# Kernel tuning notes

Hardware: AMD Instinct MI355X
Metric: run time of the kernel (lower is better)

Reference implementation:

```python
import jax, jax.numpy as jnp
import numpy as np

ADJ = (1, 3, 5)
GROUPS = 32


def band_mask(a, T):
    i = jnp.arange(T)
    return (jnp.abs(i[:, None] - i[None, :]) <= a).astype(jnp.float32)


def conv1d(x, w, b, groups=1, padding=0):
    # x: [N, C, T], w: [O, C//groups, K]
    out = jax.lax.conv_general_dilated(
        x, w, (1,), [(padding, padding)],
        dimension_numbers=('NCH', 'OIH', 'NCH'),
        feature_group_count=groups)
    return out + b[None, :, None]


def prslot_block(x, wp, bp, wk, bk, wa, ba, a):
    # x_adj = x[..., None].repeat(T) has identical columns; proj (1x1) and
    # region_key_conv (kernel (2a+1, 1)) act only along rows, so compute them
    # as 1D convs and broadcast at the mask multiply (same math as torch).
    T = x.shape[-1]
    h = conv1d(x, wp, bp)                 # [N, hid, T]
    k = conv1d(h, wk, bk, padding=a)      # [N, 128, T]
    km = k[:, :, :, None] * band_mask(a, T)  # [N, 128, T, T]
    # aggregate_conv: kernel (2a+1, 1) -> conv over rows only
    out = jax.lax.conv_general_dilated(
        km, wa[:, :, :, None], (1, 1), [(a, a), (0, 0)],
        dimension_numbers=('NCHW', 'OIHW', 'NCHW'))
    out = out[:, 0] + ba[0]               # [N, T, T]
    return jax.nn.softmax(out, axis=-2)   # softmax over rows (dim -2)


def setup_inputs() -> dict:
    key = jax.random.key(0)
    ks = iter(jax.random.split(key, 64))
    N, Cin, T = 8, 512, 192
    hid, cout = 256, 256

    def p(shape, scale):
        return jax.random.normal(next(ks), shape, jnp.float32) * scale

    d = {'x': jax.random.normal(next(ks), (N, Cin, T), jnp.float32)}
    for s, a in enumerate(ADJ):
        K = 2 * a + 1
        d[f'wp{s}'] = p((hid, Cin, 1), 0.02)
        d[f'bp{s}'] = jnp.zeros((hid,), jnp.float32)
        d[f'wk{s}'] = p((128, hid, K), 0.02)
        d[f'bk{s}'] = jnp.zeros((128,), jnp.float32)
        d[f'wa{s}'] = p((1, 128, K), 0.05)
        d[f'ba{s}'] = jnp.zeros((1,), jnp.float32)
    d['w1'] = p((hid, Cin, 1), 0.02)
    d['b1'] = jnp.zeros((hid,), jnp.float32)
    d['w2'] = p((hid, hid // GROUPS, 3), 0.05)
    d['b2'] = jnp.zeros((hid,), jnp.float32)
    d['w3'] = p((cout, hid, 1), 0.05)
    d['b3'] = jnp.zeros((cout,), jnp.float32)
    return d


def reference(x, wp0, bp0, wk0, bk0, wa0, ba0,
              wp1, bp1, wk1, bk1, wa1, ba1,
              wp2, bp2, wk2, bk2, wa2, ba2,
              w1, b1, w2, b2, w3, b3):
    scale_params = ((wp0, bp0, wk0, bk0, wa0, ba0),
                    (wp1, bp1, wk1, bk1, wa1, ba1),
                    (wp2, bp2, wk2, bk2, wa2, ba2))
    A = prslot_block(x, *scale_params[0], ADJ[0])
    A = A + prslot_block(x, *scale_params[1], ADJ[1])
    A = A + prslot_block(x, *scale_params[2], ADJ[2])  # [N, T, T]
    h = conv1d(x, w1, b1)
    h = jax.nn.relu(conv1d(h, w2, b2, groups=GROUPS, padding=1))
    xs = conv1d(h, w3, b3)                # [N, out, T]
    return xs @ A, A
```

## Files before the change

kernel.cpp:

```cpp
#include <hip/hip_runtime.h>

#define T_LEN 192

template<bool TRANSX>
__device__ __forceinline__ void gemm_body(
    float* smem,
    const float* __restrict__ W, const float* __restrict__ B,
    const float* __restrict__ X, float* __restrict__ Y,
    int cin, int cstr, int ostr, int wnstr,
    int t0, int o0, int n, int tid)
{
  float (*Ws)[68] = (float(*)[68])smem;
  float (*Xs)[68] = (float(*)[68])(smem + 64 * 68);
  const int to = tid >> 4, tt = tid & 15;
  float acc[4][4] = {};

  for (int c0 = 0; c0 < cin; c0 += 64) {
    __syncthreads();
#pragma unroll
    for (int l = 0; l < 4; ++l) {
      int idx = l * 256 + tid;
      int rr = idx >> 4, c4 = idx & 15;
      float4 wv = *reinterpret_cast<const float4*>(
          &W[(size_t)n * wnstr + (size_t)(o0 + rr) * cin + c0 + c4 * 4]);
      Ws[c4 * 4 + 0][rr] = wv.x; Ws[c4 * 4 + 1][rr] = wv.y;
      Ws[c4 * 4 + 2][rr] = wv.z; Ws[c4 * 4 + 3][rr] = wv.w;
      if (!TRANSX) {
        float4 xv = *reinterpret_cast<const float4*>(
            &X[((size_t)n * cstr + c0 + rr) * T_LEN + t0 + c4 * 4]);
        *reinterpret_cast<float4*>(&Xs[rr][c4 * 4]) = xv;
      } else {
        float4 xv = *reinterpret_cast<const float4*>(
            &X[((size_t)n * 192 + t0 + rr) * 192 + c0 + c4 * 4]);
        Xs[c4 * 4 + 0][rr] = xv.x; Xs[c4 * 4 + 1][rr] = xv.y;
        Xs[c4 * 4 + 2][rr] = xv.z; Xs[c4 * 4 + 3][rr] = xv.w;
      }
    }
    __syncthreads();
#pragma unroll
    for (int kk = 0; kk < 64; ++kk) {
      float4 a = *reinterpret_cast<const float4*>(&Ws[kk][to * 4]);
      float4 b = *reinterpret_cast<const float4*>(&Xs[kk][tt * 4]);
      acc[0][0] += a.x * b.x; acc[0][1] += a.x * b.y; acc[0][2] += a.x * b.z; acc[0][3] += a.x * b.w;
      acc[1][0] += a.y * b.x; acc[1][1] += a.y * b.y; acc[1][2] += a.y * b.z; acc[1][3] += a.y * b.w;
      acc[2][0] += a.z * b.x; acc[2][1] += a.z * b.y; acc[2][2] += a.z * b.z; acc[2][3] += a.z * b.w;
      acc[3][0] += a.w * b.x; acc[3][1] += a.w * b.y; acc[3][2] += a.w * b.z; acc[3][3] += a.w * b.w;
    }
  }
#pragma unroll
  for (int i = 0; i < 4; ++i) {
    float bi = B ? B[o0 + to * 4 + i] : 0.f;
    float4 v = make_float4(acc[i][0] + bi, acc[i][1] + bi, acc[i][2] + bi, acc[i][3] + bi);
    *reinterpret_cast<float4*>(
        &Y[((size_t)n * ostr + o0 + to * 4 + i) * T_LEN + t0 + tt * 4]) = v;
  }
}

template<int K, int JN>
__device__ __forceinline__ void foldA_body(
    const float* __restrict__ wa, const float* __restrict__ wk,
    float* __restrict__ parts, int j0, int chunk, int tid)
{
  float acc[JN][K];
#pragma unroll
  for (int jj = 0; jj < JN; ++jj)
#pragma unroll
    for (int i = 0; i < K; ++i) acc[jj][i] = 0.f;

  const int c0 = chunk * 16;
  for (int c = c0; c < c0 + 16; ++c) {
    const float* base = &wk[((size_t)c * 256 + tid) * K];
    float v[K];
#pragma unroll
    for (int i = 0; i < K; ++i) v[i] = base[i];
    float w[JN];
#pragma unroll
    for (int jj = 0; jj < JN; ++jj) w[jj] = wa[c * K + j0 + jj];
#pragma unroll
    for (int jj = 0; jj < JN; ++jj)
#pragma unroll
      for (int i = 0; i < K; ++i) acc[jj][i] += w[jj] * v[i];
  }
#pragma unroll
  for (int jj = 0; jj < JN; ++jj)
#pragma unroll
    for (int i = 0; i < K; ++i)
      parts[((size_t)chunk * K * K + (j0 + jj) * K + i) * 256 + tid] = acc[jj][i];
}

__device__ __forceinline__ void cka_body(
    const float* __restrict__ wa0, const float* __restrict__ bk0,
    const float* __restrict__ wa1, const float* __restrict__ bk1,
    const float* __restrict__ wa2, const float* __restrict__ bk2,
    float* __restrict__ cka, int tid)
{
  if (tid >= 21) return;
  int s, j, K; const float *wa, *bk;
  if (tid < 3)       { s = 0; j = tid;      K = 3;  wa = wa0; bk = bk0; }
  else if (tid < 10) { s = 1; j = tid - 3;  K = 7;  wa = wa1; bk = bk1; }
  else               { s = 2; j = tid - 10; K = 11; wa = wa2; bk = bk2; }
  float acc = 0.f;
  for (int c = 0; c < 128; ++c) acc += wa[c * K + j] * bk[c];
  cka[s * 11 + j] = acc;
}

template<int K>
__device__ __forceinline__ void foldB_body(
    float* lds, const float* __restrict__ parts, const float* __restrict__ wp,
    const float* __restrict__ bp, float* __restrict__ wxas,
    float* __restrict__ bpA_s, int ji, int half, int tid)
{
  constexpr int KP = (K + 3) & ~3;
  constexpr int K2 = K * K;
  float s = 0.f;
#pragma unroll
  for (int ch = 0; ch < 8; ++ch)
    s += parts[((size_t)(ch * K2 + ji)) * 256 + tid];
  lds[tid] = s;
  __syncthreads();

  const int cin = half * 256 + tid;
  float acc = 0.f;
  for (int c = 0; c < 256; ++c)
    acc += lds[c] * wp[(size_t)c * 512 + cin];
  const int j = ji / K, i = ji - j * K;
  wxas[(size_t)cin * K * KP + i * KP + j] = acc;

  if (half == 0 && tid == 0) {
    float b = 0.f;
    for (int c = 0; c < 256; ++c) b += lds[c] * bp[c];
    bpA_s[j * 11 + i] = b;
  }
}

template<int A>
__device__ __forceinline__ void rcomp_body(
    float* smem, const float* __restrict__ x, const float* __restrict__ WXAs,
    float* __restrict__ rps, int cc, int n, int tid)
{
  constexpr int K  = 2 * A + 1;
  constexpr int KP = (K + 3) & ~3;
  constexpr int WH = 192 + 2 * A;
  constexpr int WS = 204;
  float* Xs = smem;
  float* Wl = smem + 16 * WS;
  const int c0 = cc * 16;

  for (int idx = tid; idx < 16 * WH; idx += 256) {
    int c = idx / WH, p = idx - c * WH;
    int tau = p - A;
    Xs[c * WS + p] = (tau >= 0 && tau < 192)
        ? x[((size_t)n * 512 + c0 + c) * 192 + tau] : 0.f;
  }
  {
    const float4* wg = reinterpret_cast<const float4*>(WXAs + (size_t)c0 * K * KP);
    float4* wl = reinterpret_cast<float4*>(Wl);
    for (int idx = tid; idx < 16 * K * KP / 4; idx += 256) wl[idx] = wg[idx];
  }
  __syncthreads();

  const int w = tid >> 6, lane = tid & 63;
  const int csub = lane >> 4, tpos = lane & 15;
  const int tb = w * 48 + tpos * 3;

  float acc[K][3];
#pragma unroll
  for (int j = 0; j < K; ++j) { acc[j][0] = 0.f; acc[j][1] = 0.f; acc[j][2] = 0.f; }

#pragma unroll
  for (int c = 0; c < 4; ++c) {
    const int ch = csub * 4 + c;
    float win[K + 2];
#pragma unroll
    for (int p = 0; p < K + 2; ++p) win[p] = Xs[ch * WS + tb + p];
    const float* wr = &Wl[ch * K * KP];
#pragma unroll
    for (int i = 0; i < K; ++i) {
#pragma unroll
      for (int j = 0; j < K; ++j) {
        float wv = wr[i * KP + j];
        acc[j][0] += wv * win[i + 0];
        acc[j][1] += wv * win[i + 1];
        acc[j][2] += wv * win[i + 2];
      }
    }
  }
#pragma unroll
  for (int j = 0; j < K; ++j) {
#pragma unroll
    for (int q = 0; q < 3; ++q) {
      float v = acc[j][q];
      v += __shfl_xor(v, 16);
      v += __shfl_xor(v, 32);
      acc[j][q] = v;
    }
  }
  if (csub == 0) {
#pragma unroll
    for (int j = 0; j < K; ++j) {
      float* dst = &rps[(((size_t)n * 32 + cc) * K + j) * 192 + tb];
      dst[0] = acc[j][0]; dst[1] = acc[j][1]; dst[2] = acc[j][2];
    }
  }
}

__device__ __forceinline__ void rreduce_body(
    const float* __restrict__ rpart, const float* __restrict__ cka,
    const float* __restrict__ bpA, float* __restrict__ rbuf,
    int n, int sj, int t)
{
  if (t >= 192) return;
  const int s = sj < 3 ? 0 : sj < 10 ? 1 : 2;
  const int j = sj < 3 ? sj : sj < 10 ? sj - 3 : sj - 10;
  const int A = (s == 0) ? 1 : (s == 1) ? 3 : 5;
  const int K = 2 * A + 1;
  const int roff = (s == 0) ? 0 : (s == 1) ? 147456 : 491520;
  const float* rp = rpart + roff;
  float acc = cka[s * 11 + j];
#pragma unroll 8
  for (int cc = 0; cc < 32; ++cc)
    acc += rp[(((size_t)n * 32 + cc) * K + j) * 192 + t];
  for (int i = 0; i < K; ++i) {
    int tau = t + i - A;
    if (tau >= 0 && tau < 192) acc += bpA[s * 121 + j * 11 + i];
  }
  rbuf[((size_t)(s * 8 + n) * 11 + j) * 192 + t] = acc;
}

template<int A>
__device__ __forceinline__ float gather_val(const float* __restrict__ rs,
                                            int t, int u)
{
  constexpr int K = 2 * A + 1;
  float val = 0.f;
#pragma unroll
  for (int j = 0; j < K; ++j) {
    int tp = t + j - A;
    int d = tp - u;
    if (tp >= 0 && tp < 192 && d <= A && d >= -A) val += rs[j * 192 + tp];
  }
  return val;
}

__device__ __forceinline__ void abuild_body(
    const float* __restrict__ rbuf,
    const float* __restrict__ ba0, const float* __restrict__ ba1,
    const float* __restrict__ ba2, float* __restrict__ At,
    int ublk, int n, int tid)
{
  const int w = tid >> 6, lane = tid & 63;
  const int u = ublk * 4 + w;
  const int t0 = lane * 3;
  const float* r0 = rbuf + (size_t)(0 * 8 + n) * 11 * 192;
  const float* r1 = rbuf + (size_t)(1 * 8 + n) * 11 * 192;
  const float* r2 = rbuf + (size_t)(2 * 8 + n) * 11 * 192;
  float v0[3], v1[3], v2[3];
  const float b0 = ba0[0], b1 = ba1[0], b2 = ba2[0];
#pragma unroll
  for (int q = 0; q < 3; ++q) {
    v0[q] = b0 + gather_val<1>(r0, t0 + q, u);
    v1[q] = b1 + gather_val<3>(r1, t0 + q, u);
    v2[q] = b2 + gather_val<5>(r2, t0 + q, u);
  }
  float m0 = fmaxf(fmaxf(v0[0], v0[1]), v0[2]);
  float m1 = fmaxf(fmaxf(v1[0], v1[1]), v1[2]);
  float m2 = fmaxf(fmaxf(v2[0], v2[1]), v2[2]);
#pragma unroll
  for (int off = 32; off > 0; off >>= 1) {
    m0 = fmaxf(m0, __shfl_xor(m0, off));
    m1 = fmaxf(m1, __shfl_xor(m1, off));
    m2 = fmaxf(m2, __shfl_xor(m2, off));
  }
  float e0[3], e1[3], e2[3];
#pragma unroll
  for (int q = 0; q < 3; ++q) {
    e0[q] = __expf(v0[q] - m0);
    e1[q] = __expf(v1[q] - m1);
    e2[q] = __expf(v2[q] - m2);
  }
  float s0 = e0[0] + e0[1] + e0[2];
  float s1 = e1[0] + e1[1] + e1[2];
  float s2 = e2[0] + e2[1] + e2[2];
#pragma unroll
  for (int off = 32; off > 0; off >>= 1) {
    s0 += __shfl_xor(s0, off);
    s1 += __shfl_xor(s1, off);
    s2 += __shfl_xor(s2, off);
  }
  const float i0 = 1.f / s0, i1 = 1.f / s1, i2 = 1.f / s2;
  float* dst = &At[((size_t)n * 192 + u) * 192 + t0];
#pragma unroll
  for (int q = 0; q < 3; ++q)
    dst[q] = e0[q] * i0 + e1[q] * i1 + e2[q] * i2;
}

__device__ __forceinline__ void gconv_body(
    const float* __restrict__ hin, const float* __restrict__ w2,
    const float* __restrict__ b2, float* __restrict__ hout,
    int bx, int by, int n, int tid)
{
  const int t  = (tid & 63) + bx * 64;
  const int oc = (tid >> 6) + by * 4;
  const int g  = oc >> 3;
  float acc = b2[oc];
  for (int i = 0; i < 8; ++i) {
    const float* hrow = &hin[((size_t)n * 512 + g * 8 + i) * 192];
#pragma unroll
    for (int j = 0; j < 3; ++j) {
      int tt = t + j - 1;
      float hv = (tt >= 0 && tt < 192) ? hrow[tt] : 0.f;
      acc += w2[((size_t)oc * 8 + i) * 3 + j] * hv;
    }
  }
  hout[((size_t)n * 512 + 256 + oc) * 192 + t] = fmaxf(acc, 0.f);
}

__device__ __forceinline__ void transpose_body(
    float* smem, const float* __restrict__ At, float* __restrict__ Aout,
    int bx, int by, int n, int tid)
{
  float (*tile)[33] = (float(*)[33])smem;
  const int xx = tid & 31, y = tid >> 5;
  for (int yy = y; yy < 32; yy += 8)
    tile[yy][xx] = At[((size_t)n * 192 + by * 32 + yy) * 192 + bx * 32 + xx];
  __syncthreads();
  for (int yy = y; yy < 32; yy += 8)
    Aout[((size_t)n * 192 + bx * 32 + yy) * 192 + by * 32 + xx] = tile[xx][yy];
}

__global__ __launch_bounds__(256) void fold_a(
    const float* __restrict__ wa0, const float* __restrict__ wk0,
    const float* __restrict__ bk0,
    const float* __restrict__ wa1, const float* __restrict__ wk1,
    const float* __restrict__ bk1,
    const float* __restrict__ wa2, const float* __restrict__ wk2,
    const float* __restrict__ bk2,
    float* __restrict__ partsA, float* __restrict__ cka)
{
  const int bid = blockIdx.x, tid = threadIdx.x;
  if (bid < 48) {
    const int s = bid >> 4, sub = bid & 15;
    const int chunk = sub >> 1, jg = sub & 1;
    if (s == 0) {
      if (jg == 0) foldA_body<3, 2>(wa0, wk0, partsA,          0, chunk, tid);
      else         foldA_body<3, 1>(wa0, wk0, partsA,          2, chunk, tid);
    } else if (s == 1) {
      if (jg == 0) foldA_body<7, 4>(wa1, wk1, partsA + 18432,  0, chunk, tid);
      else         foldA_body<7, 3>(wa1, wk1, partsA + 18432,  4, chunk, tid);
    } else {
      if (jg == 0) foldA_body<11, 6>(wa2, wk2, partsA + 118784, 0, chunk, tid);
      else         foldA_body<11, 5>(wa2, wk2, partsA + 118784, 6, chunk, tid);
    }
  } else {
    cka_body(wa0, bk0, wa1, bk1, wa2, bk2, cka, tid);
  }
}

__global__ __launch_bounds__(256) void fold_b(
    const float* __restrict__ partsA,
    const float* __restrict__ wp0, const float* __restrict__ bp0,
    const float* __restrict__ wp1, const float* __restrict__ bp1,
    const float* __restrict__ wp2, const float* __restrict__ bp2,
    float* __restrict__ WXA, float* __restrict__ bpA)
{
  __shared__ float lds[256];
  const int bid = blockIdx.x, tid = threadIdx.x;
  if (bid < 18)
    foldB_body<3>(lds, partsA, wp0, bp0, WXA, bpA,
                  bid >> 1, bid & 1, tid);
  else if (bid < 116)
    foldB_body<7>(lds, partsA + 18432, wp1, bp1, WXA + 6144, bpA + 121,
                  (bid - 18) >> 1, (bid - 18) & 1, tid);
  else
    foldB_body<11>(lds, partsA + 118784, wp2, bp2, WXA + 34816, bpA + 242,
                   (bid - 116) >> 1, (bid - 116) & 1, tid);
}

__global__ __launch_bounds__(256) void k2_kernel(
    const float* __restrict__ x, const float* __restrict__ w1,
    const float* __restrict__ b1, const float* __restrict__ WXA,
    float* __restrict__ hall, float* __restrict__ rpart)
{
  __shared__ __align__(16) float smem[8704];
  const int bid = blockIdx.x, tid = threadIdx.x;
  if (bid < 96) {
    const int tx = bid % 3, oy = (bid / 3) % 4, n = bid / 12;
    gemm_body<false>(smem, w1, b1, x, hall, 512, 512, 512, 0,
                     tx * 64, oy * 64, n, tid);
  } else {
    const int rid = bid - 96;
    const int cc = rid % 32, n = (rid / 32) % 8, s = rid / 256;
    if (s == 0)      rcomp_body<1>(smem, x, WXA,         rpart,          cc, n, tid);
    else if (s == 1) rcomp_body<3>(smem, x, WXA + 6144,  rpart + 147456, cc, n, tid);
    else             rcomp_body<5>(smem, x, WXA + 34816, rpart + 491520, cc, n, tid);
  }
}

__global__ __launch_bounds__(256) void k3_kernel(
    const float* __restrict__ rpart, const float* __restrict__ cka,
    const float* __restrict__ bpA, float* __restrict__ rbuf,
    const float* __restrict__ w2, const float* __restrict__ b2,
    float* __restrict__ hall)
{
  const int bid = blockIdx.x, tid = threadIdx.x;
  if (bid < 168) {
    rreduce_body(rpart, cka, bpA, rbuf, bid % 8, bid / 8, tid);
  } else {
    const int gid = bid - 168;
    gconv_body(hall, w2, b2, hall, gid % 3, (gid / 3) % 64, gid / 192, tid);
  }
}

__global__ __launch_bounds__(256) void k4_kernel(
    const float* __restrict__ rbuf,
    const float* __restrict__ ba0, const float* __restrict__ ba1,
    const float* __restrict__ ba2, float* __restrict__ At,
    const float* __restrict__ hall, const float* __restrict__ w3,
    const float* __restrict__ b3, float* __restrict__ xs)
{
  __shared__ __align__(16) float smem[8704];
  const int bid = blockIdx.x, tid = threadIdx.x;
  if (bid < 384) {
    abuild_body(rbuf, ba0, ba1, ba2, At, bid % 48, bid / 48, tid);
  } else {
    const int gid = bid - 384;
    const int tx = gid % 3, oy = (gid / 3) % 4, n = gid / 12;
    gemm_body<false>(smem, w3, b3, hall + 256 * 192, xs, 256, 512, 256, 0,
                     tx * 64, oy * 64, n, tid);
  }
}

__global__ __launch_bounds__(256) void k5_kernel(
    const float* __restrict__ xs, const float* __restrict__ At,
    float* __restrict__ out0, float* __restrict__ Aout)
{
  __shared__ __align__(16) float smem[8704];
  const int bid = blockIdx.x, tid = threadIdx.x;
  if (bid < 96) {
    const int tx = bid % 3, oy = (bid / 3) % 4, n = bid / 12;
    gemm_body<true>(smem, xs, nullptr, At, out0, 192, 0, 256, 256 * 192,
                    tx * 64, oy * 64, n, tid);
  } else {
    const int gid = bid - 96;
    transpose_body(smem, At, Aout, gid % 6, (gid / 6) % 6, gid / 36, tid);
  }
}

extern "C" void kernel_launch(void* const* d_in, const int* in_sizes, int n_in,
                              void* d_out, int out_size, void* d_ws, size_t ws_size,
                              hipStream_t stream)
{
  const float* x   = (const float*)d_in[0];
  const float* wp0 = (const float*)d_in[1];
  const float* bp0 = (const float*)d_in[2];
  const float* wk0 = (const float*)d_in[3];
  const float* bk0 = (const float*)d_in[4];
  const float* wa0 = (const float*)d_in[5];
  const float* ba0 = (const float*)d_in[6];
  const float* wp1 = (const float*)d_in[7];
  const float* bp1 = (const float*)d_in[8];
  const float* wk1 = (const float*)d_in[9];
  const float* bk1 = (const float*)d_in[10];
  const float* wa1 = (const float*)d_in[11];
  const float* ba1 = (const float*)d_in[12];
  const float* wp2 = (const float*)d_in[13];
  const float* bp2 = (const float*)d_in[14];
  const float* wk2 = (const float*)d_in[15];
  const float* bk2 = (const float*)d_in[16];
  const float* wa2 = (const float*)d_in[17];
  const float* ba2 = (const float*)d_in[18];
  const float* w1  = (const float*)d_in[19];
  const float* b1  = (const float*)d_in[20];
  const float* w2  = (const float*)d_in[21];
  const float* b2  = (const float*)d_in[22];
  const float* w3  = (const float*)d_in[23];
  const float* b3  = (const float*)d_in[24];

  float* ws     = (float*)d_ws;
  float* hall   = ws;
  float* At     = hall   + 786432;
  float* xs     = At     + 294912;
  float* rpart  = xs     + 393216;
  float* rbuf   = rpart  + 1032192;
  float* WXA    = rbuf   + 50688;
  float* bpA    = WXA    + 102400;
  float* cka    = bpA    + 384;
  float* partsA = cka    + 64;
  float* out0   = (float*)d_out;
  float* Aout   = out0 + 8 * 256 * 192;

  fold_a<<<49, 256, 0, stream>>>(
      wa0, wk0, bk0, wa1, wk1, bk1, wa2, wk2, bk2, partsA, cka);

  fold_b<<<358, 256, 0, stream>>>(
      partsA, wp0, bp0, wp1, bp1, wp2, bp2, WXA, bpA);

  k2_kernel<<<96 + 768, 256, 0, stream>>>(x, w1, b1, WXA, hall, rpart);

  k3_kernel<<<168 + 1536, 256, 0, stream>>>(rpart, cka, bpA, rbuf, w2, b2, hall);

  k4_kernel<<<384 + 96, 256, 0, stream>>>(rbuf, ba0, ba1, ba2, At,
                                          hall, w3, b3, xs);

  k5_kernel<<<96 + 288, 256, 0, stream>>>(xs, At, out0, Aout);
}
```

Measured before the change: 81.49 us.

## Reschedule kernel stages and fuse channel reduction into softmax A-build

Moves the w1 GEMM into the first launch alongside the weight folding, runs the grouped conv with the second fold stage, and pairs the region compute with the w3 GEMM. The separate reduction kernel is removed: each A-build block now reduces its own window of rpart into shared memory before computing the banded softmax. This cuts one launch and the rbuf round trip through global memory. In exchange, neighbouring blocks redundantly re-reduce overlapping windows of rpart.

```diff
diff --git a/kernel.cpp b/kernel.cpp
--- a/kernel.cpp
+++ b/kernel.cpp
@@ -204,96 +204,6 @@
   }
 }
 
-__device__ __forceinline__ void rreduce_body(
-    const float* __restrict__ rpart, const float* __restrict__ cka,
-    const float* __restrict__ bpA, float* __restrict__ rbuf,
-    int n, int sj, int t)
-{
-  if (t >= 192) return;
-  const int s = sj < 3 ? 0 : sj < 10 ? 1 : 2;
-  const int j = sj < 3 ? sj : sj < 10 ? sj - 3 : sj - 10;
-  const int A = (s == 0) ? 1 : (s == 1) ? 3 : 5;
-  const int K = 2 * A + 1;
-  const int roff = (s == 0) ? 0 : (s == 1) ? 147456 : 491520;
-  const float* rp = rpart + roff;
-  float acc = cka[s * 11 + j];
-#pragma unroll 8
-  for (int cc = 0; cc < 32; ++cc)
-    acc += rp[(((size_t)n * 32 + cc) * K + j) * 192 + t];
-  for (int i = 0; i < K; ++i) {
-    int tau = t + i - A;
-    if (tau >= 0 && tau < 192) acc += bpA[s * 121 + j * 11 + i];
-  }
-  rbuf[((size_t)(s * 8 + n) * 11 + j) * 192 + t] = acc;
-}
-
-template<int A>
-__device__ __forceinline__ float gather_val(const float* __restrict__ rs,
-                                            int t, int u)
-{
-  constexpr int K = 2 * A + 1;
-  float val = 0.f;
-#pragma unroll
-  for (int j = 0; j < K; ++j) {
-    int tp = t + j - A;
-    int d = tp - u;
-    if (tp >= 0 && tp < 192 && d <= A && d >= -A) val += rs[j * 192 + tp];
-  }
-  return val;
-}
-
-__device__ __forceinline__ void abuild_body(
-    const float* __restrict__ rbuf,
-    const float* __restrict__ ba0, const float* __restrict__ ba1,
-    const float* __restrict__ ba2, float* __restrict__ At,
-    int ublk, int n, int tid)
-{
-  const int w = tid >> 6, lane = tid & 63;
-  const int u = ublk * 4 + w;
-  const int t0 = lane * 3;
-  const float* r0 = rbuf + (size_t)(0 * 8 + n) * 11 * 192;
-  const float* r1 = rbuf + (size_t)(1 * 8 + n) * 11 * 192;
-  const float* r2 = rbuf + (size_t)(2 * 8 + n) * 11 * 192;
-  float v0[3], v1[3], v2[3];
-  const float b0 = ba0[0], b1 = ba1[0], b2 = ba2[0];
-#pragma unroll
-  for (int q = 0; q < 3; ++q) {
-    v0[q] = b0 + gather_val<1>(r0, t0 + q, u);
-    v1[q] = b1 + gather_val<3>(r1, t0 + q, u);
-    v2[q] = b2 + gather_val<5>(r2, t0 + q, u);
-  }
-  float m0 = fmaxf(fmaxf(v0[0], v0[1]), v0[2]);
-  float m1 = fmaxf(fmaxf(v1[0], v1[1]), v1[2]);
-  float m2 = fmaxf(fmaxf(v2[0], v2[1]), v2[2]);
-#pragma unroll
-  for (int off = 32; off > 0; off >>= 1) {
-    m0 = fmaxf(m0, __shfl_xor(m0, off));
-    m1 = fmaxf(m1, __shfl_xor(m1, off));
-    m2 = fmaxf(m2, __shfl_xor(m2, off));
-  }
-  float e0[3], e1[3], e2[3];
-#pragma unroll
-  for (int q = 0; q < 3; ++q) {
-    e0[q] = __expf(v0[q] - m0);
-    e1[q] = __expf(v1[q] - m1);
-    e2[q] = __expf(v2[q] - m2);
-  }
-  float s0 = e0[0] + e0[1] + e0[2];
-  float s1 = e1[0] + e1[1] + e1[2];
-  float s2 = e2[0] + e2[1] + e2[2];
-#pragma unroll
-  for (int off = 32; off > 0; off >>= 1) {
-    s0 += __shfl_xor(s0, off);
-    s1 += __shfl_xor(s1, off);
-    s2 += __shfl_xor(s2, off);
-  }
-  const float i0 = 1.f / s0, i1 = 1.f / s1, i2 = 1.f / s2;
-  float* dst = &At[((size_t)n * 192 + u) * 192 + t0];
-#pragma unroll
-  for (int q = 0; q < 3; ++q)
-    dst[q] = e0[q] * i0 + e1[q] * i1 + e2[q] * i2;
-}
-
 __device__ __forceinline__ void gconv_body(
     const float* __restrict__ hin, const float* __restrict__ w2,
     const float* __restrict__ b2, float* __restrict__ hout,
@@ -328,18 +238,27 @@
     Aout[((size_t)n * 192 + bx * 32 + yy) * 192 + by * 32 + xx] = tile[xx][yy];
 }
 
-__global__ __launch_bounds__(256) void fold_a(
+__global__ __launch_bounds__(256) void k1_kernel(
+    const float* __restrict__ x, const float* __restrict__ w1,
+    const float* __restrict__ b1,
     const float* __restrict__ wa0, const float* __restrict__ wk0,
     const float* __restrict__ bk0,
     const float* __restrict__ wa1, const float* __restrict__ wk1,
     const float* __restrict__ bk1,
     const float* __restrict__ wa2, const float* __restrict__ wk2,
     const float* __restrict__ bk2,
-    float* __restrict__ partsA, float* __restrict__ cka)
-{
+    float* __restrict__ hall, float* __restrict__ partsA,
+    float* __restrict__ cka)
+{
+  __shared__ __align__(16) float smem[8704];
   const int bid = blockIdx.x, tid = threadIdx.x;
-  if (bid < 48) {
-    const int s = bid >> 4, sub = bid & 15;
+  if (bid < 96) {
+    const int tx = bid % 3, oy = (bid / 3) % 4, n = bid / 12;
+    gemm_body<false>(smem, w1, b1, x, hall, 512, 512, 512, 0,
+                     tx * 64, oy * 64, n, tid);
+  } else if (bid < 144) {
+    const int fbid = bid - 96;
+    const int s = fbid >> 4, sub = fbid & 15;
     const int chunk = sub >> 1, jg = sub & 1;
     if (s == 0) {
       if (jg == 0) foldA_body<3, 2>(wa0, wk0, partsA,          0, chunk, tid);
@@ -356,12 +275,14 @@
   }
 }
 
-__global__ __launch_bounds__(256) void fold_b(
+__global__ __launch_bounds__(256) void k2_kernel(
     const float* __restrict__ partsA,
     const float* __restrict__ wp0, const float* __restrict__ bp0,
     const float* __restrict__ wp1, const float* __restrict__ bp1,
     const float* __restrict__ wp2, const float* __restrict__ bp2,
-    float* __restrict__ WXA, float* __restrict__ bpA)
+    float* __restrict__ WXA, float* __restrict__ bpA,
+    const float* __restrict__ w2, const float* __restrict__ b2,
+    float* __restrict__ hall)
 {
   __shared__ float lds[256];
   const int bid = blockIdx.x, tid = threadIdx.x;
@@ -371,63 +292,133 @@
   else if (bid < 116)
     foldB_body<7>(lds, partsA + 18432, wp1, bp1, WXA + 6144, bpA + 121,
                   (bid - 18) >> 1, (bid - 18) & 1, tid);
-  else
+  else if (bid < 358)
     foldB_body<11>(lds, partsA + 118784, wp2, bp2, WXA + 34816, bpA + 242,
                    (bid - 116) >> 1, (bid - 116) & 1, tid);
-}
-
-__global__ __launch_bounds__(256) void k2_kernel(
-    const float* __restrict__ x, const float* __restrict__ w1,
-    const float* __restrict__ b1, const float* __restrict__ WXA,
-    float* __restrict__ hall, float* __restrict__ rpart)
+  else {
+    const int gid = bid - 358;
+    gconv_body(hall, w2, b2, hall, gid % 3, (gid / 3) % 64, gid / 192, tid);
+  }
+}
+
+__global__ __launch_bounds__(256) void k3_kernel(
+    const float* __restrict__ x, const float* __restrict__ WXA,
+    float* __restrict__ rpart,
+    const float* __restrict__ hall, const float* __restrict__ w3,
+    const float* __restrict__ b3, float* __restrict__ xs)
 {
   __shared__ __align__(16) float smem[8704];
   const int bid = blockIdx.x, tid = threadIdx.x;
-  if (bid < 96) {
-    const int tx = bid % 3, oy = (bid / 3) % 4, n = bid / 12;
-    gemm_body<false>(smem, w1, b1, x, hall, 512, 512, 512, 0,
-                     tx * 64, oy * 64, n, tid);
-  } else {
-    const int rid = bid - 96;
-    const int cc = rid % 32, n = (rid / 32) % 8, s = rid / 256;
+  if (bid < 768) {
+    const int cc = bid % 32, n = (bid / 32) % 8, s = bid / 256;
     if (s == 0)      rcomp_body<1>(smem, x, WXA,         rpart,          cc, n, tid);
     else if (s == 1) rcomp_body<3>(smem, x, WXA + 6144,  rpart + 147456, cc, n, tid);
     else             rcomp_body<5>(smem, x, WXA + 34816, rpart + 491520, cc, n, tid);
-  }
-}
-
-__global__ __launch_bounds__(256) void k3_kernel(
-    const float* __restrict__ rpart, const float* __restrict__ cka,
-    const float* __restrict__ bpA, float* __restrict__ rbuf,
-    const float* __restrict__ w2, const float* __restrict__ b2,
-    float* __restrict__ hall)
-{
-  const int bid = blockIdx.x, tid = threadIdx.x;
-  if (bid < 168) {
-    rreduce_body(rpart, cka, bpA, rbuf, bid % 8, bid / 8, tid);
   } else {
-    const int gid = bid - 168;
-    gconv_body(hall, w2, b2, hall, gid % 3, (gid / 3) % 64, gid / 192, tid);
-  }
-}
-
-__global__ __launch_bounds__(256) void k4_kernel(
-    const float* __restrict__ rbuf,
-    const float* __restrict__ ba0, const float* __restrict__ ba1,
-    const float* __restrict__ ba2, float* __restrict__ At,
-    const float* __restrict__ hall, const float* __restrict__ w3,
-    const float* __restrict__ b3, float* __restrict__ xs)
-{
-  __shared__ __align__(16) float smem[8704];
-  const int bid = blockIdx.x, tid = threadIdx.x;
-  if (bid < 384) {
-    abuild_body(rbuf, ba0, ba1, ba2, At, bid % 48, bid / 48, tid);
-  } else {
-    const int gid = bid - 384;
+    const int gid = bid - 768;
     const int tx = gid % 3, oy = (gid / 3) % 4, n = gid / 12;
     gemm_body<false>(smem, w3, b3, hall + 256 * 192, xs, 256, 512, 256, 0,
                      tx * 64, oy * 64, n, tid);
   }
+}
+
+__global__ __launch_bounds__(256) void k4_kernel(
+    const float* __restrict__ rpart, const float* __restrict__ cka,
+    const float* __restrict__ bpA,
+    const float* __restrict__ ba0, const float* __restrict__ ba1,
+    const float* __restrict__ ba2, float* __restrict__ At)
+{
+  __shared__ float rbW[264];
+  const int ublk = blockIdx.x % 48, n = blockIdx.x / 48;
+  const int u0 = ublk * 4;
+  const int tid = threadIdx.x;
+
+  for (int idx = tid; idx < 264; idx += 256) {
+    int s, j, w;
+    if (idx < 18)      { s = 0; j = idx / 6;  w = idx - j * 6; }
+    else if (idx < 88) { int r = idx - 18; s = 1; j = r / 10; w = r - j * 10; }
+    else               { int r = idx - 88; s = 2; j = r / 16; w = r - j * 16; }
+    const int As = (s == 0) ? 1 : (s == 1) ? 3 : 5;
+    const int Ks = 2 * As + 1;
+    const int tp = u0 - As + w;
+    float acc = 0.f;
+    if (tp >= 0 && tp < 192) {
+      acc = cka[s * 11 + j];
+      const int roff = (s == 0) ? 0 : (s == 1) ? 147456 : 491520;
+      const float* rp = rpart + roff + ((size_t)(n * 32) * Ks + j) * 192 + tp;
+      const size_t cstride = (size_t)Ks * 192;
+#pragma unroll 8
+      for (int cc = 0; cc < 32; ++cc)
+        acc += rp[cc * cstride];
+      for (int i = 0; i < Ks; ++i) {
+        int tau = tp + i - As;
+        if (tau >= 0 && tau < 192) acc += bpA[s * 121 + j * 11 + i];
+      }
+    }
+    rbW[idx] = acc;
+  }
+  __syncthreads();
+
+  const int w = tid >> 6, lane = tid & 63;
+  const int u = u0 + w;
+  const int t0 = lane * 3;
+  const float b0 = ba0[0], b1 = ba1[0], b2 = ba2[0];
+  float v0[3], v1[3], v2[3];
+#pragma unroll
+  for (int q = 0; q < 3; ++q) {
+    const int t = t0 + q;
+    float a0 = b0, a1 = b1, a2 = b2;
+#pragma unroll
+    for (int j = 0; j < 3; ++j) {
+      int tp = t + j - 1, d = tp - u;
+      if (tp >= 0 && tp < 192 && d <= 1 && d >= -1)
+        a0 += rbW[j * 6 + (t + j - u0)];
+    }
+#pragma unroll
+    for (int j = 0; j < 7; ++j) {
+      int tp = t + j - 3, d = tp - u;
+      if (tp >= 0 && tp < 192 && d <= 3 && d >= -3)
+        a1 += rbW[18 + j * 10 + (t + j - u0)];
+    }
+#pragma unroll
+    for (int j = 0; j < 11; ++j) {
+      int tp = t + j - 5, d = tp - u;
+      if (tp >= 0 && tp < 192 && d <= 5 && d >= -5)
+        a2 += rbW[88 + j * 16 + (t + j - u0)];
+    }
+    v0[q] = a0; v1[q] = a1; v2[q] = a2;
+  }
+
+  float m0 = fmaxf(fmaxf(v0[0], v0[1]), v0[2]);
+  float m1 = fmaxf(fmaxf(v1[0], v1[1]), v1[2]);
+  float m2 = fmaxf(fmaxf(v2[0], v2[1]), v2[2]);
+#pragma unroll
+  for (int off = 32; off > 0; off >>= 1) {
+    m0 = fmaxf(m0, __shfl_xor(m0, off));
+    m1 = fmaxf(m1, __shfl_xor(m1, off));
+    m2 = fmaxf(m2, __shfl_xor(m2, off));
+  }
+  float e0[3], e1[3], e2[3];
+#pragma unroll
+  for (int q = 0; q < 3; ++q) {
+    e0[q] = __expf(v0[q] - m0);
+    e1[q] = __expf(v1[q] - m1);
+    e2[q] = __expf(v2[q] - m2);
+  }
+  float s0 = e0[0] + e0[1] + e0[2];
+  float s1 = e1[0] + e1[1] + e1[2];
+  float s2 = e2[0] + e2[1] + e2[2];
+#pragma unroll
+  for (int off = 32; off > 0; off >>= 1) {
+    s0 += __shfl_xor(s0, off);
+    s1 += __shfl_xor(s1, off);
+    s2 += __shfl_xor(s2, off);
+  }
+  const float i0 = 1.f / s0, i1 = 1.f / s1, i2 = 1.f / s2;
+  float* dst = &At[((size_t)n * 192 + u) * 192 + t0];
+#pragma unroll
+  for (int q = 0; q < 3; ++q)
+    dst[q] = e0[q] * i0 + e1[q] * i1 + e2[q] * i2;
 }
 
 __global__ __launch_bounds__(256) void k5_kernel(
@@ -481,26 +472,23 @@
   float* At     = hall   + 786432;
   float* xs     = At     + 294912;
   float* rpart  = xs     + 393216;
-  float* rbuf   = rpart  + 1032192;
-  float* WXA    = rbuf   + 50688;
+  float* WXA    = rpart  + 1032192;
   float* bpA    = WXA    + 102400;
   float* cka    = bpA    + 384;
   float* partsA = cka    + 64;
   float* out0   = (float*)d_out;
   float* Aout   = out0 + 8 * 256 * 192;
 
-  fold_a<<<49, 256, 0, stream>>>(
-      wa0, wk0, bk0, wa1, wk1, bk1, wa2, wk2, bk2, partsA, cka);
-
-  fold_b<<<358, 256, 0, stream>>>(
-      partsA, wp0, bp0, wp1, bp1, wp2, bp2, WXA, bpA);
-
-  k2_kernel<<<96 + 768, 256, 0, stream>>>(x, w1, b1, WXA, hall, rpart);
-
-  k3_kernel<<<168 + 1536, 256, 0, stream>>>(rpart, cka, bpA, rbuf, w2, b2, hall);
-
-  k4_kernel<<<384 + 96, 256, 0, stream>>>(rbuf, ba0, ba1, ba2, At,
-                                          hall, w3, b3, xs);
+  k1_kernel<<<145, 256, 0, stream>>>(
+      x, w1, b1, wa0, wk0, bk0, wa1, wk1, bk1, wa2, wk2, bk2,
+      hall, partsA, cka);
+
+  k2_kernel<<<358 + 1536, 256, 0, stream>>>(
+      partsA, wp0, bp0, wp1, bp1, wp2, bp2, WXA, bpA, w2, b2, hall);
+
+  k3_kernel<<<768 + 96, 256, 0, stream>>>(x, WXA, rpart, hall, w3, b3, xs);
+
+  k4_kernel<<<384, 256, 0, stream>>>(rpart, cka, bpA, ba0, ba1, ba2, At);
 
   k5_kernel<<<96 + 288, 256, 0, stream>>>(xs, At, out0, Aout);
 }
```

New measurement: 88.63 us. +8.8%, slower.

## Compute per-scale projections directly instead of folding wp into key-aggregate weights

Applied to the files above, without the earlier changes.

Drops the fold_b stage, which folded the projection weights wp into the combined key/aggregate weights. The three scale projections (and w1) now run as one batched GEMM over x, writing hs. The region partial sums then convolve hs over 256 channels rather than x over 512, summing the 8 partsA chunks on the fly from a transposed layout. This removes one kernel launch and halves the rcomp channel reduction, but it stores three extra 256x192 hidden maps per sample and reorders the stages (abuild becomes its own kernel).

```diff
diff --git a/kernel.cpp b/kernel.cpp
--- a/kernel.cpp
+++ b/kernel.cpp
@@ -85,7 +85,7 @@
   for (int jj = 0; jj < JN; ++jj)
 #pragma unroll
     for (int i = 0; i < K; ++i)
-      parts[((size_t)chunk * K * K + (j0 + jj) * K + i) * 256 + tid] = acc[jj][i];
+      parts[((size_t)((j0 + jj) * K + i) * 256 + tid) * 8 + chunk] = acc[jj][i];
 }
 
 __device__ __forceinline__ void cka_body(
@@ -104,39 +104,11 @@
   cka[s * 11 + j] = acc;
 }
 
-template<int K>
-__device__ __forceinline__ void foldB_body(
-    float* lds, const float* __restrict__ parts, const float* __restrict__ wp,
-    const float* __restrict__ bp, float* __restrict__ wxas,
-    float* __restrict__ bpA_s, int ji, int half, int tid)
-{
-  constexpr int KP = (K + 3) & ~3;
-  constexpr int K2 = K * K;
-  float s = 0.f;
-#pragma unroll
-  for (int ch = 0; ch < 8; ++ch)
-    s += parts[((size_t)(ch * K2 + ji)) * 256 + tid];
-  lds[tid] = s;
-  __syncthreads();
-
-  const int cin = half * 256 + tid;
-  float acc = 0.f;
-  for (int c = 0; c < 256; ++c)
-    acc += lds[c] * wp[(size_t)c * 512 + cin];
-  const int j = ji / K, i = ji - j * K;
-  wxas[(size_t)cin * K * KP + i * KP + j] = acc;
-
-  if (half == 0 && tid == 0) {
-    float b = 0.f;
-    for (int c = 0; c < 256; ++c) b += lds[c] * bp[c];
-    bpA_s[j * 11 + i] = b;
-  }
-}
-
 template<int A>
-__device__ __forceinline__ void rcomp_body(
-    float* smem, const float* __restrict__ x, const float* __restrict__ WXAs,
-    float* __restrict__ rps, int cc, int n, int tid)
+__device__ __forceinline__ void rcompk_body(
+    float* smem, const float* __restrict__ hs_s,
+    const float* __restrict__ parts_s, float* __restrict__ rps,
+    int cc, int n, int tid)
 {
   constexpr int K  = 2 * A + 1;
   constexpr int KP = (K + 3) & ~3;
@@ -150,12 +122,16 @@
     int c = idx / WH, p = idx - c * WH;
     int tau = p - A;
     Xs[c * WS + p] = (tau >= 0 && tau < 192)
-        ? x[((size_t)n * 512 + c0 + c) * 192 + tau] : 0.f;
-  }
-  {
-    const float4* wg = reinterpret_cast<const float4*>(WXAs + (size_t)c0 * K * KP);
-    float4* wl = reinterpret_cast<float4*>(Wl);
-    for (int idx = tid; idx < 16 * K * KP / 4; idx += 256) wl[idx] = wg[idx];
+        ? hs_s[((size_t)n * 768 + c0 + c) * 192 + tau] : 0.f;
+  }
+  for (int idx = tid; idx < 16 * K * K; idx += 256) {
+    int ji = idx >> 4, c = idx & 15;
+    const float* p = &parts_s[((size_t)ji * 256 + c0 + c) * 8];
+    float4 a = *reinterpret_cast<const float4*>(p);
+    float4 b = *reinterpret_cast<const float4*>(p + 4);
+    float wsum = (a.x + a.y + a.z + a.w) + (b.x + b.y + b.z + b.w);
+    int j = ji / K, i = ji - j * K;
+    Wl[c * K * KP + i * KP + j] = wsum;
   }
   __syncthreads();
 
@@ -198,7 +174,7 @@
   if (csub == 0) {
 #pragma unroll
     for (int j = 0; j < K; ++j) {
-      float* dst = &rps[(((size_t)n * 32 + cc) * K + j) * 192 + tb];
+      float* dst = &rps[(((size_t)n * 16 + cc) * K + j) * 192 + tb];
       dst[0] = acc[j][0]; dst[1] = acc[j][1]; dst[2] = acc[j][2];
     }
   }
@@ -206,24 +182,18 @@
 
 __device__ __forceinline__ void rreduce_body(
     const float* __restrict__ rpart, const float* __restrict__ cka,
-    const float* __restrict__ bpA, float* __restrict__ rbuf,
-    int n, int sj, int t)
+    float* __restrict__ rbuf, int n, int sj, int t)
 {
   if (t >= 192) return;
   const int s = sj < 3 ? 0 : sj < 10 ? 1 : 2;
   const int j = sj < 3 ? sj : sj < 10 ? sj - 3 : sj - 10;
-  const int A = (s == 0) ? 1 : (s == 1) ? 3 : 5;
-  const int K = 2 * A + 1;
-  const int roff = (s == 0) ? 0 : (s == 1) ? 147456 : 491520;
+  const int K = (s == 0) ? 3 : (s == 1) ? 7 : 11;
+  const int roff = (s == 0) ? 0 : (s == 1) ? 73728 : 245760;
   const float* rp = rpart + roff;
   float acc = cka[s * 11 + j];
 #pragma unroll 8
-  for (int cc = 0; cc < 32; ++cc)
-    acc += rp[(((size_t)n * 32 + cc) * K + j) * 192 + t];
-  for (int i = 0; i < K; ++i) {
-    int tau = t + i - A;
-    if (tau >= 0 && tau < 192) acc += bpA[s * 121 + j * 11 + i];
-  }
+  for (int cc = 0; cc < 16; ++cc)
+    acc += rp[(((size_t)n * 16 + cc) * K + j) * 192 + t];
   rbuf[((size_t)(s * 8 + n) * 11 + j) * 192 + t] = acc;
 }
 
@@ -328,18 +298,35 @@
     Aout[((size_t)n * 192 + bx * 32 + yy) * 192 + by * 32 + xx] = tile[xx][yy];
 }
 
-__global__ __launch_bounds__(256) void fold_a(
+__global__ __launch_bounds__(256) void p1_kernel(
+    const float* __restrict__ x,
+    const float* __restrict__ wp0, const float* __restrict__ bp0,
+    const float* __restrict__ wp1, const float* __restrict__ bp1,
+    const float* __restrict__ wp2, const float* __restrict__ bp2,
+    const float* __restrict__ w1, const float* __restrict__ b1,
     const float* __restrict__ wa0, const float* __restrict__ wk0,
     const float* __restrict__ bk0,
     const float* __restrict__ wa1, const float* __restrict__ wk1,
     const float* __restrict__ bk1,
     const float* __restrict__ wa2, const float* __restrict__ wk2,
     const float* __restrict__ bk2,
+    float* __restrict__ hs, float* __restrict__ hall,
     float* __restrict__ partsA, float* __restrict__ cka)
 {
+  __shared__ __align__(16) float smem[8704];
   const int bid = blockIdx.x, tid = threadIdx.x;
-  if (bid < 48) {
-    const int s = bid >> 4, sub = bid & 15;
+  if (bid < 384) {
+    const int proj = bid / 96, gid = bid % 96;
+    const int tx = gid % 3, oy = (gid / 3) % 4, n = gid / 12;
+    const float* W = proj == 0 ? wp0 : proj == 1 ? wp1 : proj == 2 ? wp2 : w1;
+    const float* B = proj == 0 ? bp0 : proj == 1 ? bp1 : proj == 2 ? bp2 : b1;
+    float* Y  = proj < 3 ? hs + (size_t)proj * 256 * 192 : hall;
+    int ostr  = proj < 3 ? 768 : 512;
+    gemm_body<false>(smem, W, B, x, Y, 512, 512, ostr, 0,
+                     tx * 64, oy * 64, n, tid);
+  } else if (bid < 432) {
+    const int fbid = bid - 384;
+    const int s = fbid >> 4, sub = fbid & 15;
     const int chunk = sub >> 1, jg = sub & 1;
     if (s == 0) {
       if (jg == 0) foldA_body<3, 2>(wa0, wk0, partsA,          0, chunk, tid);
@@ -356,81 +343,56 @@
   }
 }
 
-__global__ __launch_bounds__(256) void fold_b(
-    const float* __restrict__ partsA,
-    const float* __restrict__ wp0, const float* __restrict__ bp0,
-    const float* __restrict__ wp1, const float* __restrict__ bp1,
-    const float* __restrict__ wp2, const float* __restrict__ bp2,
-    float* __restrict__ WXA, float* __restrict__ bpA)
-{
-  __shared__ float lds[256];
+__global__ __launch_bounds__(256) void p2_kernel(
+    const float* __restrict__ hs, const float* __restrict__ partsA,
+    float* __restrict__ rpart,
+    const float* __restrict__ w2, const float* __restrict__ b2,
+    float* __restrict__ hall)
+{
+  __shared__ __align__(16) float smem[5440];
   const int bid = blockIdx.x, tid = threadIdx.x;
-  if (bid < 18)
-    foldB_body<3>(lds, partsA, wp0, bp0, WXA, bpA,
-                  bid >> 1, bid & 1, tid);
-  else if (bid < 116)
-    foldB_body<7>(lds, partsA + 18432, wp1, bp1, WXA + 6144, bpA + 121,
-                  (bid - 18) >> 1, (bid - 18) & 1, tid);
-  else
-    foldB_body<11>(lds, partsA + 118784, wp2, bp2, WXA + 34816, bpA + 242,
-                   (bid - 116) >> 1, (bid - 116) & 1, tid);
-}
-
-__global__ __launch_bounds__(256) void k2_kernel(
-    const float* __restrict__ x, const float* __restrict__ w1,
-    const float* __restrict__ b1, const float* __restrict__ WXA,
-    float* __restrict__ hall, float* __restrict__ rpart)
+  if (bid < 384) {
+    const int cc = bid % 16, n = (bid / 16) % 8, s = bid / 128;
+    if (s == 0)
+      rcompk_body<1>(smem, hs,                 partsA,          rpart,          cc, n, tid);
+    else if (s == 1)
+      rcompk_body<3>(smem, hs + 256 * 192,     partsA + 18432,  rpart + 73728,  cc, n, tid);
+    else
+      rcompk_body<5>(smem, hs + 512 * 192,     partsA + 118784, rpart + 245760, cc, n, tid);
+  } else {
+    const int gid = bid - 384;
+    gconv_body(hall, w2, b2, hall, gid % 3, (gid / 3) % 64, gid / 192, tid);
+  }
+}
+
+__global__ __launch_bounds__(256) void p3_kernel(
+    const float* __restrict__ rpart, const float* __restrict__ cka,
+    float* __restrict__ rbuf,
+    const float* __restrict__ hall, const float* __restrict__ w3,
+    const float* __restrict__ b3, float* __restrict__ xs)
 {
   __shared__ __align__(16) float smem[8704];
   const int bid = blockIdx.x, tid = threadIdx.x;
-  if (bid < 96) {
-    const int tx = bid % 3, oy = (bid / 3) % 4, n = bid / 12;
-    gemm_body<false>(smem, w1, b1, x, hall, 512, 512, 512, 0,
-                     tx * 64, oy * 64, n, tid);
-  } else {
-    const int rid = bid - 96;
-    const int cc = rid % 32, n = (rid / 32) % 8, s = rid / 256;
-    if (s == 0)      rcomp_body<1>(smem, x, WXA,         rpart,          cc, n, tid);
-    else if (s == 1) rcomp_body<3>(smem, x, WXA + 6144,  rpart + 147456, cc, n, tid);
-    else             rcomp_body<5>(smem, x, WXA + 34816, rpart + 491520, cc, n, tid);
-  }
-}
-
-__global__ __launch_bounds__(256) void k3_kernel(
-    const float* __restrict__ rpart, const float* __restrict__ cka,
-    const float* __restrict__ bpA, float* __restrict__ rbuf,
-    const float* __restrict__ w2, const float* __restrict__ b2,
-    float* __restrict__ hall)
-{
-  const int bid = blockIdx.x, tid = threadIdx.x;
   if (bid < 168) {
-    rreduce_body(rpart, cka, bpA, rbuf, bid % 8, bid / 8, tid);
+    rreduce_body(rpart, cka, rbuf, bid % 8, bid / 8, tid);
   } else {
     const int gid = bid - 168;
-    gconv_body(hall, w2, b2, hall, gid % 3, (gid / 3) % 64, gid / 192, tid);
-  }
-}
-
-__global__ __launch_bounds__(256) void k4_kernel(
-    const float* __restrict__ rbuf,
-    const float* __restrict__ ba0, const float* __restrict__ ba1,
-    const float* __restrict__ ba2, float* __restrict__ At,
-    const float* __restrict__ hall, const float* __restrict__ w3,
-    const float* __restrict__ b3, float* __restrict__ xs)
-{
-  __shared__ __align__(16) float smem[8704];
-  const int bid = blockIdx.x, tid = threadIdx.x;
-  if (bid < 384) {
-    abuild_body(rbuf, ba0, ba1, ba2, At, bid % 48, bid / 48, tid);
-  } else {
-    const int gid = bid - 384;
     const int tx = gid % 3, oy = (gid / 3) % 4, n = gid / 12;
     gemm_body<false>(smem, w3, b3, hall + 256 * 192, xs, 256, 512, 256, 0,
                      tx * 64, oy * 64, n, tid);
   }
 }
 
-__global__ __launch_bounds__(256) void k5_kernel(
+__global__ __launch_bounds__(256) void p4_kernel(
+    const float* __restrict__ rbuf,
+    const float* __restrict__ ba0, const float* __restrict__ ba1,
+    const float* __restrict__ ba2, float* __restrict__ At)
+{
+  abuild_body(rbuf, ba0, ba1, ba2, At, blockIdx.x % 48, blockIdx.x / 48,
+              threadIdx.x);
+}
+
+__global__ __launch_bounds__(256) void p5_kernel(
     const float* __restrict__ xs, const float* __restrict__ At,
     float* __restrict__ out0, float* __restrict__ Aout)
 {
@@ -478,29 +440,26 @@
 
   float* ws     = (float*)d_ws;
   float* hall   = ws;
-  float* At     = hall   + 786432;
+  float* hs     = hall   + 786432;
+  float* At     = hs     + 1179648;
   float* xs     = At     + 294912;
   float* rpart  = xs     + 393216;
-  float* rbuf   = rpart  + 1032192;
-  float* WXA    = rbuf   + 50688;
-  float* bpA    = WXA    + 102400;
-  float* cka    = bpA    + 384;
+  float* rbuf   = rpart  + 516096;
+  float* cka    = rbuf   + 50688;
   float* partsA = cka    + 64;
   float* out0   = (float*)d_out;
   float* Aout   = out0 + 8 * 256 * 192;
 
-  fold_a<<<49, 256, 0, stream>>>(
-      wa0, wk0, bk0, wa1, wk1, bk1, wa2, wk2, bk2, partsA, cka);
-
-  fold_b<<<358, 256, 0, stream>>>(
-      partsA, wp0, bp0, wp1, bp1, wp2, bp2, WXA, bpA);
-
-  k2_kernel<<<96 + 768, 256, 0, stream>>>(x, w1, b1, WXA, hall, rpart);
-
-  k3_kernel<<<168 + 1536, 256, 0, stream>>>(rpart, cka, bpA, rbuf, w2, b2, hall);
-
-  k4_kernel<<<384 + 96, 256, 0, stream>>>(rbuf, ba0, ba1, ba2, At,
-                                          hall, w3, b3, xs);
-
-  k5_kernel<<<96 + 288, 256, 0, stream>>>(xs, At, out0, Aout);
-}
+  p1_kernel<<<433, 256, 0, stream>>>(
+      x, wp0, bp0, wp1, bp1, wp2, bp2, w1, b1,
+      wa0, wk0, bk0, wa1, wk1, bk1, wa2, wk2, bk2,
+      hs, hall, partsA, cka);
+
+  p2_kernel<<<384 + 1536, 256, 0, stream>>>(hs, partsA, rpart, w2, b2, hall);
+
+  p3_kernel<<<168 + 96, 256, 0, stream>>>(rpart, cka, rbuf, hall, w3, b3, xs);
+
+  p4_kernel<<<384, 256, 0, stream>>>(rbuf, ba0, ba1, ba2, At);
+
+  p5_kernel<<<96 + 288, 256, 0, stream>>>(xs, At, out0, Aout);
+}
```

New measurement: 90.35 us. +10.9%, slower.
